# Optimization experiments

Hardware: AMD Instinct MI355X
Metric: run time of the kernel (lower is better)

## Reference

```python
import jax, jax.numpy as jnp
import numpy as np

PATCH = 16  # conv kernel size == stride


def _patch_embed(im, W, b):
    # im: (B, C, H, W) NCHW; W: (hidden, C, s, s); returns (B, h, w, hidden)
    out = jax.lax.conv_general_dilated(
        im, W, window_strides=(PATCH, PATCH), padding='VALID',
        dimension_numbers=('NCHW', 'OIHW', 'NCHW'))
    out = out + b[None, :, None, None]
    return jnp.transpose(out, (0, 2, 3, 1))  # (B, h, w, hidden)


def setup_inputs() -> dict:
    key = jax.random.key(0)
    k1, k2, k3, k4 = jax.random.split(key, 4)
    B, C, H, Wd = 64, 3, 224, 224
    hidden = 384
    x = jax.random.normal(k1, (B, C, H, Wd), dtype=jnp.float32)
    y = jax.random.normal(k2, (B, C, H, Wd), dtype=jnp.float32)
    fan_in = C * PATCH * PATCH
    bound = 1.0 / np.sqrt(fan_in)
    W = jax.random.uniform(k3, (hidden, C, PATCH, PATCH), dtype=jnp.float32,
                           minval=-bound, maxval=bound)
    b = jax.random.uniform(k4, (hidden,), dtype=jnp.float32,
                           minval=-bound, maxval=bound)
    return {'x': x, 'y': y, 'W': W, 'b': b}


def reference(x, y, W, b):
    B = x.shape[0]
    xp = _patch_embed(x, W, b)  # (B, h, w, C)
    yp = _patch_embed(y, W, b)  # (B, h, w, C)
    h, w = xp.shape[1], xp.shape[2]
    logp = jax.nn.log_softmax(xp, axis=-1)          # (B, h, w, C)
    q = jax.lax.stop_gradient(jax.nn.softmax(yp, axis=-1))  # detached targets
    # CE[i, j] = mean over (h, w) of -(q_j * logp_i).sum(-1)
    # Faithful factorization of the (B, B, h, w, C) broadcast in the original.
    CE = -jnp.einsum('ihwc,jhwc->ij', logp, q) / (h * w)  # (B, B)
    close = jnp.trace(CE) / B
    far = (CE.sum() - jnp.trace(CE)) / (B * B - B)
    return close / far
```

## Files before the change

### kernel.cpp

```cpp
#include <hip/hip_runtime.h>

#define HID   384
#define K_PE  768
#define IMGST 150528
#define NCOLS 75264

typedef unsigned short ushort_t;
using f32x4  = __attribute__((ext_vector_type(4))) float;
using short8 = __attribute__((ext_vector_type(8))) short;

__device__ __forceinline__ unsigned bfpack(float lo, float hi) {
    union { float f; unsigned u; } a, b; a.f = lo; b.f = hi;
    unsigned ra = (a.u + 0x7fffu + ((a.u >> 16) & 1u)) >> 16;
    unsigned rb = (b.u + 0x7fffu + ((b.u >> 16) & 1u)) & 0xffff0000u;
    return ra | rb;
}

__global__ __launch_bounds__(256) void prep(const float* __restrict__ W,
                                            ushort_t* __restrict__ Wfrag,
                                            float* __restrict__ scal,
                                            float* __restrict__ Lsum,
                                            float* __restrict__ Qsum) {
    const int t = blockIdx.x * 256 + threadIdx.x;
    if (t < 4) scal[t] = 0.f;
    if (t < NCOLS / 4) {
        ((float4*)Lsum)[t] = float4{0.f, 0.f, 0.f, 0.f};
        ((float4*)Qsum)[t] = float4{0.f, 0.f, 0.f, 0.f};
    }
    if (t < 36864) {
        const int n  = t / 96;
        const int ko = t % 96;
        const float4 a = *(const float4*)(W + (size_t)n * K_PE + ko * 8);
        const float4 b = *(const float4*)(W + (size_t)n * K_PE + ko * 8 + 4);
        uint4 p;
        p.x = bfpack(a.x, a.y); p.y = bfpack(a.z, a.w);
        p.z = bfpack(b.x, b.y); p.w = bfpack(b.z, b.w);
        const int nt   = n >> 4;
        const int kc   = ko >> 2;
        const int lane = (ko & 3) * 16 + (n & 15);
        ((uint4*)Wfrag)[(nt * 24 + kc) * 64 + lane] = p;
    }
}

__global__ __launch_bounds__(256, 3) void pe_all(
    const float* __restrict__ xin, const float* __restrict__ yin,
    const ushort_t* __restrict__ Wfrag, const float* __restrict__ bias,
    float* __restrict__ scal, float* __restrict__ Lsum,
    float* __restrict__ Qsum) {
    const int p  = blockIdx.x;
    const int ig = blockIdx.y;
    const int pi = p / 14;
    const int pj = p - pi * 14;

    __shared__ __align__(16) ushort_t As[2][16 * 768];
    __shared__ float Smx[4][16], Ssx[4][16], Smy[4][16], Ssy[4][16];
    __shared__ float sT[4];

    const int tid  = threadIdx.x;
    const int wave = tid >> 6;
    const int lane = tid & 63;
    const int lm   = lane & 15;
    const int lq   = lane >> 4;
    const int wn   = wave * 96;

    {
        const int z    = tid >> 7;
        const int tt   = tid & 127;
        const int simg = tt >> 3;
        const int qt   = tt & 7;
        const float* ab = (z ? yin : xin) +
                          (size_t)(ig * 16 + simg) * IMGST + pi * 3584 + pj * 16;
        ushort_t* lb = &As[z][simg * 768];
#pragma unroll
        for (int j = 0; j < 6; ++j) {
            const int rr = qt + j * 8;
            const float* ap = ab + (rr >> 4) * 50176 + (rr & 15) * 224;
            float4 f0 = *(const float4*)(ap);
            float4 f1 = *(const float4*)(ap + 4);
            float4 f2 = *(const float4*)(ap + 8);
            float4 f3 = *(const float4*)(ap + 12);
            uint4 p0, p1;
            p0.x = bfpack(f0.x, f0.y); p0.y = bfpack(f0.z, f0.w);
            p0.z = bfpack(f1.x, f1.y); p0.w = bfpack(f1.z, f1.w);
            p1.x = bfpack(f2.x, f2.y); p1.y = bfpack(f2.z, f2.w);
            p1.z = bfpack(f3.x, f3.y); p1.w = bfpack(f3.z, f3.w);
            const int c0 = rr * 2;
            *(uint4*)&lb[((c0    ) ^ (simg & 7)) * 8] = p0;
            *(uint4*)&lb[((c0 + 1) ^ (simg & 7)) * 8] = p1;
        }
    }

    const ushort_t* bbase = Wfrag + (size_t)lane * 8;
    f32x4 accx[6] = {};
    f32x4 accy[6] = {};

    __syncthreads();

#pragma unroll
    for (int kbi = 0; kbi < 12; ++kbi) {
#pragma unroll
        for (int ks = 0; ks < 2; ++ks) {
            short8 bfr[6];
#pragma unroll
            for (int ni = 0; ni < 6; ++ni)
                bfr[ni] = *(const short8*)(bbase +
                          (size_t)(((wave * 6 + ni) * 24 + kbi * 2 + ks) * 64) * 8);
            const int aoff = lm * 768 +
                             (kbi * 8 + ((ks * 4 + lq) ^ (lm & 7))) * 8;
            short8 afx = *(const short8*)&As[0][aoff];
            short8 afy = *(const short8*)&As[1][aoff];
#pragma unroll
            for (int ni = 0; ni < 6; ++ni) {
                accx[ni] = __builtin_amdgcn_mfma_f32_16x16x32_bf16(
                    afx, bfr[ni], accx[ni], 0, 0, 0);
                accy[ni] = __builtin_amdgcn_mfma_f32_16x16x32_bf16(
                    afy, bfr[ni], accy[ni], 0, 0, 0);
            }
        }
    }

#pragma unroll
    for (int ni = 0; ni < 6; ++ni) {
        const float bv = bias[wn + ni * 16 + lm];
#pragma unroll
        for (int r = 0; r < 4; ++r) {
            accx[ni][r] += bv;
            accy[ni][r] += bv;
        }
    }

    float mx[4], my_[4];
#pragma unroll
    for (int r = 0; r < 4; ++r) {
        float a = accx[0][r], b = accy[0][r];
#pragma unroll
        for (int ni = 1; ni < 6; ++ni) {
            a = fmaxf(a, accx[ni][r]);
            b = fmaxf(b, accy[ni][r]);
        }
        mx[r] = a; my_[r] = b;
    }
#pragma unroll
    for (int off = 1; off < 16; off <<= 1)
#pragma unroll
        for (int r = 0; r < 4; ++r) {
            mx[r]  = fmaxf(mx[r],  __shfl_xor(mx[r],  off));
            my_[r] = fmaxf(my_[r], __shfl_xor(my_[r], off));
        }
    if (lm == 0)
#pragma unroll
        for (int r = 0; r < 4; ++r) {
            Smx[wave][lq * 4 + r] = mx[r];
            Smy[wave][lq * 4 + r] = my_[r];
        }
    __syncthreads();
#pragma unroll
    for (int r = 0; r < 4; ++r) {
        const int row = lq * 4 + r;
        mx[r]  = fmaxf(fmaxf(Smx[0][row], Smx[1][row]),
                       fmaxf(Smx[2][row], Smx[3][row]));
        my_[r] = fmaxf(fmaxf(Smy[0][row], Smy[1][row]),
                       fmaxf(Smy[2][row], Smy[3][row]));
    }

    float sx[4], sy[4];
#pragma unroll
    for (int r = 0; r < 4; ++r) {
        float a = 0.f, b = 0.f;
#pragma unroll
        for (int ni = 0; ni < 6; ++ni) {
            a += __expf(accx[ni][r] - mx[r]);
            b += __expf(accy[ni][r] - my_[r]);
        }
        sx[r] = a; sy[r] = b;
    }
#pragma unroll
    for (int off = 1; off < 16; off <<= 1)
#pragma unroll
        for (int r = 0; r < 4; ++r) {
            sx[r] += __shfl_xor(sx[r], off);
            sy[r] += __shfl_xor(sy[r], off);
        }
    if (lm == 0)
#pragma unroll
        for (int r = 0; r < 4; ++r) {
            Ssx[wave][lq * 4 + r] = sx[r];
            Ssy[wave][lq * 4 + r] = sy[r];
        }
    __syncthreads();
#pragma unroll
    for (int r = 0; r < 4; ++r) {
        const int row = lq * 4 + r;
        const float ssx = Ssx[0][row] + Ssx[1][row] + Ssx[2][row] + Ssx[3][row];
        const float ssy = Ssy[0][row] + Ssy[1][row] + Ssy[2][row] + Ssy[3][row];
        sx[r] = mx[r] + __logf(ssx);
        sy[r] = 1.f / ssy;
    }

    float T = 0.f;
    float cL[6], cQ[6];
#pragma unroll
    for (int ni = 0; ni < 6; ++ni) { cL[ni] = 0.f; cQ[ni] = 0.f; }
#pragma unroll
    for (int r = 0; r < 4; ++r) {
        const float sh  = sx[r];
        const float m   = my_[r];
        const float inv = sy[r];
#pragma unroll
        for (int ni = 0; ni < 6; ++ni) {
            const float lp = accx[ni][r] - sh;
            const float qv = __expf(accy[ni][r] - m) * inv;
            T += lp * qv;
            cL[ni] += lp;
            cQ[ni] += qv;
        }
    }
#pragma unroll
    for (int ni = 0; ni < 6; ++ni) {
        cL[ni] += __shfl_xor(cL[ni], 16); cL[ni] += __shfl_xor(cL[ni], 32);
        cQ[ni] += __shfl_xor(cQ[ni], 16); cQ[ni] += __shfl_xor(cQ[ni], 32);
    }
    if (lq == 0)
#pragma unroll
        for (int ni = 0; ni < 6; ++ni) {
            const int col = p * HID + wn + ni * 16 + lm;
            atomicAdd(&Lsum[col], cL[ni]);
            atomicAdd(&Qsum[col], cQ[ni]);
        }
#pragma unroll
    for (int off = 32; off > 0; off >>= 1) T += __shfl_xor(T, off);
    if (lane == 0) sT[wave] = T;
    __syncthreads();
    if (tid == 0)
        atomicAdd(&scal[0], sT[0] + sT[1] + sT[2] + sT[3]);
}

__global__ __launch_bounds__(256) void final_dot(const float* __restrict__ Lsum,
                                                 const float* __restrict__ Qsum,
                                                 float* __restrict__ scal,
                                                 float* __restrict__ out) {
    const int idx = blockIdx.x * 256 + threadIdx.x;
    float s = 0.f;
    if (idx < NCOLS / 4) {
        float4 a = ((const float4*)Lsum)[idx];
        float4 b = ((const float4*)Qsum)[idx];
        s = a.x * b.x + a.y * b.y + a.z * b.z + a.w * b.w;
    }
#pragma unroll
    for (int off = 32; off > 0; off >>= 1) s += __shfl_xor(s, off);
    __shared__ float sS[4];
    __shared__ int lastflag;
    if ((threadIdx.x & 63) == 0) sS[threadIdx.x >> 6] = s;
    __syncthreads();
    if (threadIdx.x == 0) {
        atomicAdd(&scal[1], sS[0] + sS[1] + sS[2] + sS[3]);
        __threadfence();
        int old = atomicAdd((int*)&scal[3], 1);
        lastflag = (old == (int)gridDim.x - 1);
    }
    __syncthreads();
    if (lastflag && threadIdx.x == 0) {
        float S = atomicAdd(&scal[1], 0.f);
        float T = atomicAdd(&scal[0], 0.f);
        out[0] = 63.f * T / (S - T);
    }
}

extern "C" void kernel_launch(void* const* d_in, const int* in_sizes, int n_in,
                              void* d_out, int out_size, void* d_ws, size_t ws_size,
                              hipStream_t stream) {
    const float* x = (const float*)d_in[0];
    const float* y = (const float*)d_in[1];
    const float* W = (const float*)d_in[2];
    const float* b = (const float*)d_in[3];
    float* out = (float*)d_out;

    float*    scal  = (float*)d_ws;
    float*    Lsum  = scal + 16;
    float*    Qsum  = Lsum + NCOLS;
    ushort_t* Wfrag = (ushort_t*)(Qsum + NCOLS);

    prep<<<148, 256, 0, stream>>>(W, Wfrag, scal, Lsum, Qsum);
    pe_all<<<dim3(196, 4), 256, 0, stream>>>(x, y, Wfrag, b, scal, Lsum, Qsum);
    final_dot<<<74, 256, 0, stream>>>(Lsum, Qsum, scal, out);
}
```

Baseline: 164.4 us.

## Pre-convert patches to swizzled bf16 buffer and stream into LDS via global_load_lds

Moves the fp32-to-bf16 conversion and patch im2col out of the GEMM kernel into the prep kernel, which writes a pre-swizzled bf16 patch matrix to workspace. The GEMM kernel then fills shared memory with direct global-to-LDS 16-byte loads, with no register staging or conversion. The aim is to shorten the GEMM prologue and use better-coalesced loads. In exchange it adds a full write and re-read of a bf16 copy of both inputs (about 38 MB) through global memory, plus a much larger prep launch.

After: 164.6 us. Within noise of the previous version (+0.1%).

```diff
diff --git a/kernel.cpp b/kernel.cpp
--- a/kernel.cpp
+++ b/kernel.cpp
@@ -4,6 +4,7 @@
 #define K_PE  768
 #define IMGST 150528
 #define NCOLS 75264
+#define XPHALF 9633792
 
 typedef unsigned short ushort_t;
 using f32x4  = __attribute__((ext_vector_type(4))) float;
@@ -16,11 +17,17 @@
     return ra | rb;
 }
 
-__global__ __launch_bounds__(256) void prep(const float* __restrict__ W,
-                                            ushort_t* __restrict__ Wfrag,
-                                            float* __restrict__ scal,
-                                            float* __restrict__ Lsum,
-                                            float* __restrict__ Qsum) {
+__device__ __forceinline__ void gl_lds16(const void* g, void* l) {
+    __builtin_amdgcn_global_load_lds(
+        (const __attribute__((address_space(1))) unsigned*)g,
+        (__attribute__((address_space(3))) unsigned*)l, 16, 0, 0);
+}
+
+__global__ __launch_bounds__(256) void pe_prep(
+    const float* __restrict__ x, const float* __restrict__ y,
+    const float* __restrict__ W, ushort_t* __restrict__ Wfrag,
+    ushort_t* __restrict__ Xp, float* __restrict__ scal,
+    float* __restrict__ Lsum, float* __restrict__ Qsum) {
     const int t = blockIdx.x * 256 + threadIdx.x;
     if (t < 4) scal[t] = 0.f;
     if (t < NCOLS / 4) {
@@ -32,25 +39,42 @@
         const int ko = t % 96;
         const float4 a = *(const float4*)(W + (size_t)n * K_PE + ko * 8);
         const float4 b = *(const float4*)(W + (size_t)n * K_PE + ko * 8 + 4);
-        uint4 p;
-        p.x = bfpack(a.x, a.y); p.y = bfpack(a.z, a.w);
-        p.z = bfpack(b.x, b.y); p.w = bfpack(b.z, b.w);
+        uint4 pk;
+        pk.x = bfpack(a.x, a.y); pk.y = bfpack(a.z, a.w);
+        pk.z = bfpack(b.x, b.y); pk.w = bfpack(b.z, b.w);
         const int nt   = n >> 4;
         const int kc   = ko >> 2;
         const int lane = (ko & 3) * 16 + (n & 15);
-        ((uint4*)Wfrag)[(nt * 24 + kc) * 64 + lane] = p;
-    }
-}
-
-__global__ __launch_bounds__(256, 3) void pe_all(
-    const float* __restrict__ xin, const float* __restrict__ yin,
-    const ushort_t* __restrict__ Wfrag, const float* __restrict__ bias,
-    float* __restrict__ scal, float* __restrict__ Lsum,
-    float* __restrict__ Qsum) {
+        ((uint4*)Wfrag)[(nt * 24 + kc) * 64 + lane] = pk;
+    }
+    const int o = t % 96;
+    int rest    = t / 96;
+    const int i = rest & 63;
+    rest >>= 6;
+    const int p = rest % 196;
+    const int z = rest / 196;
+    const int c    = o >> 5;
+    const int di   = (o >> 1) & 15;
+    const int half = o & 1;
+    const int pi   = p / 14;
+    const int pj   = p - pi * 14;
+    const float* src = (z ? y : x) +
+        ((size_t)(i * 3 + c) * 224 + pi * 16 + di) * 224 + pj * 16 + half * 8;
+    float4 f0 = *(const float4*)src;
+    float4 f1 = *(const float4*)(src + 4);
+    uint4 pk;
+    pk.x = bfpack(f0.x, f0.y); pk.y = bfpack(f0.z, f0.w);
+    pk.z = bfpack(f1.x, f1.y); pk.w = bfpack(f1.z, f1.w);
+    const int op = (o & ~7) | ((o & 7) ^ (i & 7));
+    ((uint4*)Xp)[(size_t)z * 1204224 + (size_t)(p * 64 + i) * 96 + op] = pk;
+}
+
+__global__ __launch_bounds__(256, 3) void pe_gemm(
+    const ushort_t* __restrict__ Xp, const ushort_t* __restrict__ Wfrag,
+    const float* __restrict__ bias, float* __restrict__ scal,
+    float* __restrict__ Lsum, float* __restrict__ Qsum) {
     const int p  = blockIdx.x;
     const int ig = blockIdx.y;
-    const int pi = p / 14;
-    const int pj = p - pi * 14;
 
     __shared__ __align__(16) ushort_t As[2][16 * 768];
     __shared__ float Smx[4][16], Ssx[4][16], Smy[4][16], Ssy[4][16];
@@ -64,29 +88,13 @@
     const int wn   = wave * 96;
 
     {
-        const int z    = tid >> 7;
-        const int tt   = tid & 127;
-        const int simg = tt >> 3;
-        const int qt   = tt & 7;
-        const float* ab = (z ? yin : xin) +
-                          (size_t)(ig * 16 + simg) * IMGST + pi * 3584 + pj * 16;
-        ushort_t* lb = &As[z][simg * 768];
-#pragma unroll
-        for (int j = 0; j < 6; ++j) {
-            const int rr = qt + j * 8;
-            const float* ap = ab + (rr >> 4) * 50176 + (rr & 15) * 224;
-            float4 f0 = *(const float4*)(ap);
-            float4 f1 = *(const float4*)(ap + 4);
-            float4 f2 = *(const float4*)(ap + 8);
-            float4 f3 = *(const float4*)(ap + 12);
-            uint4 p0, p1;
-            p0.x = bfpack(f0.x, f0.y); p0.y = bfpack(f0.z, f0.w);
-            p0.z = bfpack(f1.x, f1.y); p0.w = bfpack(f1.z, f1.w);
-            p1.x = bfpack(f2.x, f2.y); p1.y = bfpack(f2.z, f2.w);
-            p1.z = bfpack(f3.x, f3.y); p1.w = bfpack(f3.z, f3.w);
-            const int c0 = rr * 2;
-            *(uint4*)&lb[((c0    ) ^ (simg & 7)) * 8] = p0;
-            *(uint4*)&lb[((c0 + 1) ^ (simg & 7)) * 8] = p1;
+        const ushort_t* xs = Xp + (size_t)(p * 64 + ig * 16) * 768;
+        const ushort_t* ys = xs + XPHALF;
+#pragma unroll
+        for (int c6 = 0; c6 < 6; ++c6) {
+            const int ch = wave * 6 + c6;
+            gl_lds16(xs + (size_t)ch * 512 + lane * 8, &As[0][ch * 512]);
+            gl_lds16(ys + (size_t)ch * 512 + lane * 8, &As[1][ch * 512]);
         }
     }
 
@@ -279,8 +287,9 @@
     float*    Lsum  = scal + 16;
     float*    Qsum  = Lsum + NCOLS;
     ushort_t* Wfrag = (ushort_t*)(Qsum + NCOLS);
-
-    prep<<<148, 256, 0, stream>>>(W, Wfrag, scal, Lsum, Qsum);
-    pe_all<<<dim3(196, 4), 256, 0, stream>>>(x, y, Wfrag, b, scal, Lsum, Qsum);
+    ushort_t* Xp    = Wfrag + 294912;
+
+    pe_prep<<<9408, 256, 0, stream>>>(x, y, W, Wfrag, Xp, scal, Lsum, Qsum);
+    pe_gemm<<<dim3(196, 4), 256, 0, stream>>>(Xp, Wfrag, b, scal, Lsum, Qsum);
     final_dot<<<74, 256, 0, stream>>>(Lsum, Qsum, scal, out);
 }
```
